# Optimization experiments

Measured on AMD Instinct MI355X. Metric: run time of the kernel, lower is better.

## Reference

```python
import jax, jax.numpy as jnp
import numpy as np

B, T, N_EMBED, HEAD_SIZE = 512, 256, 384, 64

def setup_inputs() -> dict:
    key = jax.random.key(0)
    k1, k2, k3, k4 = jax.random.split(key, 4)
    x = jax.random.normal(k1, (B, T, N_EMBED), dtype=jnp.float32)
    # nn.Linear(n_embed, head_size, bias=False) weights, stored as [in, out] for x @ W
    scale = 1.0 / np.sqrt(N_EMBED)
    Wk = jax.random.uniform(k2, (N_EMBED, HEAD_SIZE), jnp.float32, -scale, scale)
    Wq = jax.random.uniform(k3, (N_EMBED, HEAD_SIZE), jnp.float32, -scale, scale)
    Wv = jax.random.uniform(k4, (N_EMBED, HEAD_SIZE), jnp.float32, -scale, scale)
    return {"x": x, "Wk": Wk, "Wq": Wq, "Wv": Wv}

def reference(x, Wk, Wq, Wv):
    # Single causal self-attention head (dropout in eval mode / identity)
    k = x @ Wk  # [B, T, H]
    q = x @ Wq
    v = x @ Wv
    wei = jnp.einsum('bth,bsh->bts', q, k) * (HEAD_SIZE ** -0.5)  # [B, T, T]
    causal = jnp.tril(jnp.ones((T, T), dtype=bool))
    wei = jnp.where(causal, wei, -jnp.inf)
    wei = jax.nn.softmax(wei, axis=-1)
    out = jnp.einsum('bts,bsh->bth', wei, v)  # [B, T, H]
    return out
```

## Files before the change

### kernel.cpp

```cpp
#include <hip/hip_runtime.h>
#include <stdint.h>


typedef short s16x8 __attribute__((ext_vector_type(8)));
typedef float f32x4 __attribute__((ext_vector_type(4)));

#define LOG2E_OVER_8 0.18033688011112042f

__device__ inline short f2bf(float f) {
  union { float f; uint32_t u; } v; v.f = f;
  uint32_t r = (v.u + 0x7fffu + ((v.u >> 16) & 1u)) >> 16;
  return (short)r;
}

__global__ __launch_bounds__(256) void prep_w(const float* __restrict__ Wk,
                                              const float* __restrict__ Wq,
                                              const float* __restrict__ Wv,
                                              short* __restrict__ Wt2) {
  int idx = blockIdx.x * 256 + threadIdx.x;
  int kk = idx & 31;
  int n = (idx >> 5) % 192;
  int kc = idx / (32 * 192);
  int col = n & 63;
  int w = n >> 6;
  const float* W = (w == 0) ? Wk : (w == 1) ? Wq : Wv;
  float v = W[(kc * 32 + kk) * 64 + col];
  if (w == 1) v *= LOG2E_OVER_8;
  Wt2[idx] = f2bf(v);
}

__global__ __launch_bounds__(256) void qkv_proj(const float* __restrict__ x,
                                                const short* __restrict__ Wt2,
                                                short* __restrict__ Kd,
                                                short* __restrict__ Qd,
                                                short* __restrict__ Vd) {
  __shared__ short Xs[128 * 56];
  __shared__ short Ws[192 * 32];
  const int tid = threadIdx.x;
  const int wave = tid >> 6;
  const int lane = tid & 63;
  const int l15 = lane & 15;
  const int quad = lane >> 4;
  const long m0 = (long)blockIdx.x * 128;

  f32x4 acc[2][12];
#pragma unroll
  for (int mt = 0; mt < 2; ++mt)
#pragma unroll
    for (int n = 0; n < 12; ++n) acc[mt][n] = (f32x4)0.0f;

  const int xrow = tid >> 1;
  const int xcb = (tid & 1) * 16;
  const float* xp0 = x + (m0 + xrow) * 384 + xcb;
  const short* wp0 = Wt2 + tid * 24;
  short* xs = &Xs[xrow * 56 + xcb];
  short* wsp = &Ws[tid * 24];

  for (int kc = 0; kc < 12; ++kc) {
    const float* xp = xp0 + kc * 32;
    f32x4 a0 = *(const f32x4*)(xp);
    f32x4 a1 = *(const f32x4*)(xp + 4);
    f32x4 a2 = *(const f32x4*)(xp + 8);
    f32x4 a3 = *(const f32x4*)(xp + 12);
    const short* wp = wp0 + kc * 6144;
    s16x8 w0 = *(const s16x8*)(wp);
    s16x8 w1 = *(const s16x8*)(wp + 8);
    s16x8 w2 = *(const s16x8*)(wp + 16);

    s16x8 v0, v1;
    v0[0] = f2bf(a0[0]); v0[1] = f2bf(a0[1]); v0[2] = f2bf(a0[2]); v0[3] = f2bf(a0[3]);
    v0[4] = f2bf(a1[0]); v0[5] = f2bf(a1[1]); v0[6] = f2bf(a1[2]); v0[7] = f2bf(a1[3]);
    v1[0] = f2bf(a2[0]); v1[1] = f2bf(a2[1]); v1[2] = f2bf(a2[2]); v1[3] = f2bf(a2[3]);
    v1[4] = f2bf(a3[0]); v1[5] = f2bf(a3[1]); v1[6] = f2bf(a3[2]); v1[7] = f2bf(a3[3]);
    *(s16x8*)xs = v0;
    *(s16x8*)(xs + 8) = v1;
    *(s16x8*)wsp = w0;
    *(s16x8*)(wsp + 8) = w1;
    *(s16x8*)(wsp + 16) = w2;
    __syncthreads();

    s16x8 af0 = *(const s16x8*)&Xs[(wave * 32 + l15) * 56 + quad * 8];
    s16x8 af1 = *(const s16x8*)&Xs[(wave * 32 + 16 + l15) * 56 + quad * 8];
#pragma unroll
    for (int n = 0; n < 12; ++n) {
      s16x8 bf = *(const s16x8*)&Ws[(n * 16 + l15) * 32 + quad * 8];
      acc[0][n] = __builtin_amdgcn_mfma_f32_16x16x32_bf16(af0, bf, acc[0][n], 0, 0, 0);
      acc[1][n] = __builtin_amdgcn_mfma_f32_16x16x32_bf16(af1, bf, acc[1][n], 0, 0, 0);
    }
    __syncthreads();
  }

#pragma unroll
  for (int mt = 0; mt < 2; ++mt) {
    const long rbase = m0 + wave * 32 + mt * 16 + quad * 4;
#pragma unroll
    for (int n = 0; n < 12; ++n) {
      short* dst = (n < 4) ? Kd : (n < 8) ? Qd : Vd;
      const int col = (n & 3) * 16 + l15;
#pragma unroll
      for (int r = 0; r < 4; ++r) {
        dst[(rbase + r) * 64 + col] = f2bf(acc[mt][n][r]);
      }
    }
  }
}

__global__ __launch_bounds__(256) void attn_head(const short* __restrict__ Kd,
                                                 const short* __restrict__ Qd,
                                                 const short* __restrict__ Vd,
                                                 float* __restrict__ out) {
  __shared__ short Ks[64 * 72];
  __shared__ short Vt[64 * 72];
  __shared__ short Ps[4][16 * 72];
  const int tid = threadIdx.x;
  const int wave = tid >> 6;
  const int lane = tid & 63;
  const int l15 = lane & 15;
  const int quad = lane >> 4;
  const int b = blockIdx.x >> 2;
  const int qt = blockIdx.x & 3;
  const short* Kb = Kd + (long)b * (256 * 64);
  const short* Vb = Vd + (long)b * (256 * 64);
  const short* Qb = Qd + (long)b * (256 * 64);

  const int qrow = qt * 64 + wave * 16 + l15;
  s16x8 qf0 = *(const s16x8*)&Qb[qrow * 64 + quad * 8];
  s16x8 qf1 = *(const s16x8*)&Qb[qrow * 64 + 32 + quad * 8];

  f32x4 Oacc[4];
#pragma unroll
  for (int n = 0; n < 4; ++n) Oacc[n] = (f32x4)0.0f;
  float mrow[4] = {-1e30f, -1e30f, -1e30f, -1e30f};
  float lrow[4] = {0.f, 0.f, 0.f, 0.f};

  const int s_row = tid >> 2;
  const int hseg = (tid & 3) * 16;

  for (int c = 0; c <= qt; ++c) {
    const short* kp = Kb + (c * 64 + s_row) * 64 + hseg;
    s16x8 k0 = *(const s16x8*)kp;
    s16x8 k1 = *(const s16x8*)(kp + 8);
    const short* vp = Vb + (c * 64 + s_row) * 64 + hseg;
    s16x8 u0 = *(const s16x8*)vp;
    s16x8 u1 = *(const s16x8*)(vp + 8);
    *(s16x8*)&Ks[s_row * 72 + hseg] = k0;
    *(s16x8*)&Ks[s_row * 72 + hseg + 8] = k1;
#pragma unroll
    for (int i = 0; i < 8; ++i) Vt[(hseg + i) * 72 + s_row] = u0[i];
#pragma unroll
    for (int i = 0; i < 8; ++i) Vt[(hseg + 8 + i) * 72 + s_row] = u1[i];
    __syncthreads();

    f32x4 S[4];
#pragma unroll
    for (int n = 0; n < 4; ++n) {
      s16x8 kf0 = *(const s16x8*)&Ks[(n * 16 + l15) * 72 + quad * 8];
      s16x8 kf1 = *(const s16x8*)&Ks[(n * 16 + l15) * 72 + 32 + quad * 8];
      f32x4 z = (f32x4)0.0f;
      z = __builtin_amdgcn_mfma_f32_16x16x32_bf16(qf0, kf0, z, 0, 0, 0);
      z = __builtin_amdgcn_mfma_f32_16x16x32_bf16(qf1, kf1, z, 0, 0, 0);
      S[n] = z;
    }
    if (c == qt) {
#pragma unroll
      for (int n = 0; n < 4; ++n) {
        int s_loc = n * 16 + l15;
#pragma unroll
        for (int r = 0; r < 4; ++r) {
          int q_loc = wave * 16 + quad * 4 + r;
          if (s_loc > q_loc) S[n][r] = -1e30f;
        }
      }
    }

    float alpha[4];
#pragma unroll
    for (int r = 0; r < 4; ++r) {
      float mx = fmaxf(fmaxf(S[0][r], S[1][r]), fmaxf(S[2][r], S[3][r]));
      mx = fmaxf(mx, __shfl_xor(mx, 1));
      mx = fmaxf(mx, __shfl_xor(mx, 2));
      mx = fmaxf(mx, __shfl_xor(mx, 4));
      mx = fmaxf(mx, __shfl_xor(mx, 8));
      float mnew = fmaxf(mrow[r], mx);
      alpha[r] = __builtin_amdgcn_exp2f(mrow[r] - mnew);
      mrow[r] = mnew;
    }
    float rs[4] = {0.f, 0.f, 0.f, 0.f};
#pragma unroll
    for (int n = 0; n < 4; ++n) {
#pragma unroll
      for (int r = 0; r < 4; ++r) {
        float p = __builtin_amdgcn_exp2f(S[n][r] - mrow[r]);
        rs[r] += p;
        Ps[wave][(quad * 4 + r) * 72 + n * 16 + l15] = f2bf(p);
      }
    }
#pragma unroll
    for (int r = 0; r < 4; ++r) {
      float s = rs[r];
      s += __shfl_xor(s, 1);
      s += __shfl_xor(s, 2);
      s += __shfl_xor(s, 4);
      s += __shfl_xor(s, 8);
      lrow[r] = lrow[r] * alpha[r] + s;
#pragma unroll
      for (int n = 0; n < 4; ++n) Oacc[n][r] *= alpha[r];
    }
    asm volatile("s_waitcnt lgkmcnt(0)" ::: "memory");

    s16x8 pf0 = *(const s16x8*)&Ps[wave][l15 * 72 + quad * 8];
    s16x8 pf1 = *(const s16x8*)&Ps[wave][l15 * 72 + 32 + quad * 8];
#pragma unroll
    for (int n = 0; n < 4; ++n) {
      s16x8 vf0 = *(const s16x8*)&Vt[(n * 16 + l15) * 72 + quad * 8];
      s16x8 vf1 = *(const s16x8*)&Vt[(n * 16 + l15) * 72 + 32 + quad * 8];
      Oacc[n] = __builtin_amdgcn_mfma_f32_16x16x32_bf16(pf0, vf0, Oacc[n], 0, 0, 0);
      Oacc[n] = __builtin_amdgcn_mfma_f32_16x16x32_bf16(pf1, vf1, Oacc[n], 0, 0, 0);
    }
    __syncthreads();
  }

  float inv[4];
#pragma unroll
  for (int r = 0; r < 4; ++r) inv[r] = 1.0f / lrow[r];
  float* ob = out + ((long)b * 256 + qt * 64 + wave * 16 + quad * 4) * 64;
#pragma unroll
  for (int n = 0; n < 4; ++n)
#pragma unroll
    for (int r = 0; r < 4; ++r)
      ob[r * 64 + n * 16 + l15] = Oacc[n][r] * inv[r];
}

extern "C" void kernel_launch(void* const* d_in, const int* in_sizes, int n_in,
                              void* d_out, int out_size, void* d_ws, size_t ws_size,
                              hipStream_t stream) {
  const float* x = (const float*)d_in[0];
  const float* Wk = (const float*)d_in[1];
  const float* Wq = (const float*)d_in[2];
  const float* Wv = (const float*)d_in[3];
  float* out = (float*)d_out;
  char* ws = (char*)d_ws;
  short* Wt2 = (short*)ws;
  short* Kd = (short*)(ws + 147456);
  short* Qd = (short*)(ws + 147456 + 16777216);
  short* Vd = (short*)(ws + 147456 + 2 * 16777216);

  prep_w<<<288, 256, 0, stream>>>(Wk, Wq, Wv, Wt2);
  qkv_proj<<<1024, 256, 0, stream>>>(x, Wt2, Kd, Qd, Vd);
  attn_head<<<2048, 256, 0, stream>>>(Kd, Qd, Vd, out);
}
```

Before: 338.2 us.

## Fuse QKV projection and causal attention into one per-batch kernel

Replaces the separate projection and attention kernels with one kernel per batch element. It computes K, Q and a transposed V for all 256 rows into shared memory and then runs causal flash attention, pairing query tiles (t, 15-t) per wave to balance the causal work. This removes the global round trip of the bf16 K/Q/V intermediates and one kernel launch. In exchange it uses large shared memory per block, launches only 512 blocks, and reads the weight B-fragments directly from global memory instead of staging them in shared memory.

After: 357.3 us. 5.7% more time.

```diff
diff --git a/kernel.cpp b/kernel.cpp
--- a/kernel.cpp
+++ b/kernel.cpp
@@ -3,6 +3,7 @@
 
 
 typedef short s16x8 __attribute__((ext_vector_type(8)));
+typedef short s16x4 __attribute__((ext_vector_type(4)));
 typedef float f32x4 __attribute__((ext_vector_type(4)));
 
 #define LOG2E_OVER_8 0.18033688011112042f
@@ -29,206 +30,171 @@
   Wt2[idx] = f2bf(v);
 }
 
-__global__ __launch_bounds__(256) void qkv_proj(const float* __restrict__ x,
-                                                const short* __restrict__ Wt2,
-                                                short* __restrict__ Kd,
-                                                short* __restrict__ Qd,
-                                                short* __restrict__ Vd) {
-  __shared__ short Xs[128 * 56];
-  __shared__ short Ws[192 * 32];
+__global__ __launch_bounds__(512, 2) void fused_head(const float* __restrict__ x,
+                                                     const short* __restrict__ Wt2,
+                                                     float* __restrict__ out) {
+  __shared__ __align__(16) short Xs[64 * 392];
+  __shared__ __align__(16) short Kls[256 * 72];
+  __shared__ __align__(16) short Qls[256 * 72];
+  __shared__ __align__(16) short Vt[64 * 264];
+
   const int tid = threadIdx.x;
   const int wave = tid >> 6;
   const int lane = tid & 63;
   const int l15 = lane & 15;
   const int quad = lane >> 4;
-  const long m0 = (long)blockIdx.x * 128;
-
-  f32x4 acc[2][12];
-#pragma unroll
-  for (int mt = 0; mt < 2; ++mt)
-#pragma unroll
-    for (int n = 0; n < 12; ++n) acc[mt][n] = (f32x4)0.0f;
-
-  const int xrow = tid >> 1;
-  const int xcb = (tid & 1) * 16;
-  const float* xp0 = x + (m0 + xrow) * 384 + xcb;
-  const short* wp0 = Wt2 + tid * 24;
-  short* xs = &Xs[xrow * 56 + xcb];
-  short* wsp = &Ws[tid * 24];
-
-  for (int kc = 0; kc < 12; ++kc) {
-    const float* xp = xp0 + kc * 32;
-    f32x4 a0 = *(const f32x4*)(xp);
-    f32x4 a1 = *(const f32x4*)(xp + 4);
-    f32x4 a2 = *(const f32x4*)(xp + 8);
-    f32x4 a3 = *(const f32x4*)(xp + 12);
-    const short* wp = wp0 + kc * 6144;
-    s16x8 w0 = *(const s16x8*)(wp);
-    s16x8 w1 = *(const s16x8*)(wp + 8);
-    s16x8 w2 = *(const s16x8*)(wp + 16);
-
-    s16x8 v0, v1;
-    v0[0] = f2bf(a0[0]); v0[1] = f2bf(a0[1]); v0[2] = f2bf(a0[2]); v0[3] = f2bf(a0[3]);
-    v0[4] = f2bf(a1[0]); v0[5] = f2bf(a1[1]); v0[6] = f2bf(a1[2]); v0[7] = f2bf(a1[3]);
-    v1[0] = f2bf(a2[0]); v1[1] = f2bf(a2[1]); v1[2] = f2bf(a2[2]); v1[3] = f2bf(a2[3]);
-    v1[4] = f2bf(a3[0]); v1[5] = f2bf(a3[1]); v1[6] = f2bf(a3[2]); v1[7] = f2bf(a3[3]);
-    *(s16x8*)xs = v0;
-    *(s16x8*)(xs + 8) = v1;
-    *(s16x8*)wsp = w0;
-    *(s16x8*)(wsp + 8) = w1;
-    *(s16x8*)(wsp + 16) = w2;
+  const int b = blockIdx.x;
+  const float* xb = x + (long)b * (256 * 384);
+
+  const int rt = wave >> 1;
+  const int nh = wave & 1;
+  const short* wbase = Wt2 + (nh * 96 + l15) * 32 + quad * 8;
+
+  for (int ch = 0; ch < 4; ++ch) {
+    const int R0 = ch * 64;
+#pragma unroll
+    for (int j = 0; j < 12; ++j) {
+      int slot = tid + j * 512;
+      int row = slot / 96;
+      int c4 = slot - row * 96;
+      f32x4 a = *(const f32x4*)(xb + (R0 + row) * 384 + c4 * 4);
+      s16x4 h;
+      h[0] = f2bf(a[0]); h[1] = f2bf(a[1]); h[2] = f2bf(a[2]); h[3] = f2bf(a[3]);
+      *(s16x4*)&Xs[row * 392 + c4 * 4] = h;
+    }
     __syncthreads();
 
-    s16x8 af0 = *(const s16x8*)&Xs[(wave * 32 + l15) * 56 + quad * 8];
-    s16x8 af1 = *(const s16x8*)&Xs[(wave * 32 + 16 + l15) * 56 + quad * 8];
-#pragma unroll
-    for (int n = 0; n < 12; ++n) {
-      s16x8 bf = *(const s16x8*)&Ws[(n * 16 + l15) * 32 + quad * 8];
-      acc[0][n] = __builtin_amdgcn_mfma_f32_16x16x32_bf16(af0, bf, acc[0][n], 0, 0, 0);
-      acc[1][n] = __builtin_amdgcn_mfma_f32_16x16x32_bf16(af1, bf, acc[1][n], 0, 0, 0);
+    f32x4 acc[6];
+#pragma unroll
+    for (int nt = 0; nt < 6; ++nt) acc[nt] = (f32x4)0.0f;
+    const short* abase = &Xs[(rt * 16 + l15) * 392 + quad * 8];
+#pragma unroll 2
+    for (int kc = 0; kc < 12; ++kc) {
+      s16x8 af = *(const s16x8*)(abase + kc * 32);
+#pragma unroll
+      for (int nt = 0; nt < 6; ++nt) {
+        s16x8 bf = *(const s16x8*)(wbase + kc * 6144 + nt * 512);
+        acc[nt] = __builtin_amdgcn_mfma_f32_16x16x32_bf16(af, bf, acc[nt], 0, 0, 0);
+      }
+    }
+
+    const int srow = R0 + rt * 16 + quad * 4;
+#pragma unroll
+    for (int nt = 0; nt < 6; ++nt) {
+      const int gn = nh * 6 + nt;
+      if (gn < 4) {
+        const int col = gn * 16 + l15;
+#pragma unroll
+        for (int r = 0; r < 4; ++r) Kls[(srow + r) * 72 + col] = f2bf(acc[nt][r]);
+      } else if (gn < 8) {
+        const int col = (gn - 4) * 16 + l15;
+#pragma unroll
+        for (int r = 0; r < 4; ++r) Qls[(srow + r) * 72 + col] = f2bf(acc[nt][r]);
+      } else {
+        const int hcol = (gn - 8) * 16 + l15;
+#pragma unroll
+        for (int r = 0; r < 4; ++r) Vt[hcol * 264 + srow + r] = f2bf(acc[nt][r]);
+      }
     }
     __syncthreads();
   }
 
-#pragma unroll
-  for (int mt = 0; mt < 2; ++mt) {
-    const long rbase = m0 + wave * 32 + mt * 16 + quad * 4;
-#pragma unroll
-    for (int n = 0; n < 12; ++n) {
-      short* dst = (n < 4) ? Kd : (n < 8) ? Qd : Vd;
-      const int col = (n & 3) * 16 + l15;
+  short* Psw = Xs + wave * (16 * 72);
+
+  for (int ti = 0; ti < 2; ++ti) {
+    const int t = ti ? (15 - wave) : wave;
+    const int q0 = t * 16;
+
+    s16x8 qf0 = *(const s16x8*)&Qls[(q0 + l15) * 72 + quad * 8];
+    s16x8 qf1 = *(const s16x8*)&Qls[(q0 + l15) * 72 + 32 + quad * 8];
+
+    f32x4 Oacc[4];
+#pragma unroll
+    for (int n = 0; n < 4; ++n) Oacc[n] = (f32x4)0.0f;
+    float mrow[4] = {-1e30f, -1e30f, -1e30f, -1e30f};
+    float lrow[4] = {0.f, 0.f, 0.f, 0.f};
+
+    const int nchunks = (t >> 2) + 1;
+    for (int c = 0; c < nchunks; ++c) {
+      const int s0 = c * 64;
+      f32x4 S[4];
+#pragma unroll
+      for (int n = 0; n < 4; ++n) {
+        s16x8 kf0 = *(const s16x8*)&Kls[(s0 + n * 16 + l15) * 72 + quad * 8];
+        s16x8 kf1 = *(const s16x8*)&Kls[(s0 + n * 16 + l15) * 72 + 32 + quad * 8];
+        f32x4 z = (f32x4)0.0f;
+        z = __builtin_amdgcn_mfma_f32_16x16x32_bf16(qf0, kf0, z, 0, 0, 0);
+        z = __builtin_amdgcn_mfma_f32_16x16x32_bf16(qf1, kf1, z, 0, 0, 0);
+        S[n] = z;
+      }
+      if (c == nchunks - 1) {
+#pragma unroll
+        for (int n = 0; n < 4; ++n) {
+          const int s_abs = s0 + n * 16 + l15;
+#pragma unroll
+          for (int r = 0; r < 4; ++r) {
+            const int q_abs = q0 + quad * 4 + r;
+            if (s_abs > q_abs) S[n][r] = -1e30f;
+          }
+        }
+      }
+
+      float alpha[4];
 #pragma unroll
       for (int r = 0; r < 4; ++r) {
-        dst[(rbase + r) * 64 + col] = f2bf(acc[mt][n][r]);
-      }
-    }
+        float mx = fmaxf(fmaxf(S[0][r], S[1][r]), fmaxf(S[2][r], S[3][r]));
+        mx = fmaxf(mx, __shfl_xor(mx, 1));
+        mx = fmaxf(mx, __shfl_xor(mx, 2));
+        mx = fmaxf(mx, __shfl_xor(mx, 4));
+        mx = fmaxf(mx, __shfl_xor(mx, 8));
+        float mnew = fmaxf(mrow[r], mx);
+        alpha[r] = __builtin_amdgcn_exp2f(mrow[r] - mnew);
+        mrow[r] = mnew;
+      }
+      float rs[4] = {0.f, 0.f, 0.f, 0.f};
+#pragma unroll
+      for (int n = 0; n < 4; ++n) {
+#pragma unroll
+        for (int r = 0; r < 4; ++r) {
+          float p = __builtin_amdgcn_exp2f(S[n][r] - mrow[r]);
+          rs[r] += p;
+          Psw[(quad * 4 + r) * 72 + n * 16 + l15] = f2bf(p);
+        }
+      }
+#pragma unroll
+      for (int r = 0; r < 4; ++r) {
+        float s = rs[r];
+        s += __shfl_xor(s, 1);
+        s += __shfl_xor(s, 2);
+        s += __shfl_xor(s, 4);
+        s += __shfl_xor(s, 8);
+        lrow[r] = lrow[r] * alpha[r] + s;
+#pragma unroll
+        for (int n = 0; n < 4; ++n) Oacc[n][r] *= alpha[r];
+      }
+      asm volatile("s_waitcnt lgkmcnt(0)" ::: "memory");
+
+      s16x8 pf0 = *(const s16x8*)&Psw[l15 * 72 + quad * 8];
+      s16x8 pf1 = *(const s16x8*)&Psw[l15 * 72 + 32 + quad * 8];
+#pragma unroll
+      for (int n = 0; n < 4; ++n) {
+        s16x8 vf0 = *(const s16x8*)&Vt[(n * 16 + l15) * 264 + s0 + quad * 8];
+        s16x8 vf1 = *(const s16x8*)&Vt[(n * 16 + l15) * 264 + s0 + 32 + quad * 8];
+        Oacc[n] = __builtin_amdgcn_mfma_f32_16x16x32_bf16(pf0, vf0, Oacc[n], 0, 0, 0);
+        Oacc[n] = __builtin_amdgcn_mfma_f32_16x16x32_bf16(pf1, vf1, Oacc[n], 0, 0, 0);
+      }
+    }
+
+    float inv[4];
+#pragma unroll
+    for (int r = 0; r < 4; ++r) inv[r] = 1.0f / lrow[r];
+    float* ob = out + ((long)b * 256 + q0 + quad * 4) * 64;
+#pragma unroll
+    for (int n = 0; n < 4; ++n)
+#pragma unroll
+      for (int r = 0; r < 4; ++r)
+        ob[r * 64 + n * 16 + l15] = Oacc[n][r] * inv[r];
   }
-}
-
-__global__ __launch_bounds__(256) void attn_head(const short* __restrict__ Kd,
-                                                 const short* __restrict__ Qd,
-                                                 const short* __restrict__ Vd,
-                                                 float* __restrict__ out) {
-  __shared__ short Ks[64 * 72];
-  __shared__ short Vt[64 * 72];
-  __shared__ short Ps[4][16 * 72];
-  const int tid = threadIdx.x;
-  const int wave = tid >> 6;
-  const int lane = tid & 63;
-  const int l15 = lane & 15;
-  const int quad = lane >> 4;
-  const int b = blockIdx.x >> 2;
-  const int qt = blockIdx.x & 3;
-  const short* Kb = Kd + (long)b * (256 * 64);
-  const short* Vb = Vd + (long)b * (256 * 64);
-  const short* Qb = Qd + (long)b * (256 * 64);
-
-  const int qrow = qt * 64 + wave * 16 + l15;
-  s16x8 qf0 = *(const s16x8*)&Qb[qrow * 64 + quad * 8];
-  s16x8 qf1 = *(const s16x8*)&Qb[qrow * 64 + 32 + quad * 8];
-
-  f32x4 Oacc[4];
-#pragma unroll
-  for (int n = 0; n < 4; ++n) Oacc[n] = (f32x4)0.0f;
-  float mrow[4] = {-1e30f, -1e30f, -1e30f, -1e30f};
-  float lrow[4] = {0.f, 0.f, 0.f, 0.f};
-
-  const int s_row = tid >> 2;
-  const int hseg = (tid & 3) * 16;
-
-  for (int c = 0; c <= qt; ++c) {
-    const short* kp = Kb + (c * 64 + s_row) * 64 + hseg;
-    s16x8 k0 = *(const s16x8*)kp;
-    s16x8 k1 = *(const s16x8*)(kp + 8);
-    const short* vp = Vb + (c * 64 + s_row) * 64 + hseg;
-    s16x8 u0 = *(const s16x8*)vp;
-    s16x8 u1 = *(const s16x8*)(vp + 8);
-    *(s16x8*)&Ks[s_row * 72 + hseg] = k0;
-    *(s16x8*)&Ks[s_row * 72 + hseg + 8] = k1;
-#pragma unroll
-    for (int i = 0; i < 8; ++i) Vt[(hseg + i) * 72 + s_row] = u0[i];
-#pragma unroll
-    for (int i = 0; i < 8; ++i) Vt[(hseg + 8 + i) * 72 + s_row] = u1[i];
-    __syncthreads();
-
-    f32x4 S[4];
-#pragma unroll
-    for (int n = 0; n < 4; ++n) {
-      s16x8 kf0 = *(const s16x8*)&Ks[(n * 16 + l15) * 72 + quad * 8];
-      s16x8 kf1 = *(const s16x8*)&Ks[(n * 16 + l15) * 72 + 32 + quad * 8];
-      f32x4 z = (f32x4)0.0f;
-      z = __builtin_amdgcn_mfma_f32_16x16x32_bf16(qf0, kf0, z, 0, 0, 0);
-      z = __builtin_amdgcn_mfma_f32_16x16x32_bf16(qf1, kf1, z, 0, 0, 0);
-      S[n] = z;
-    }
-    if (c == qt) {
-#pragma unroll
-      for (int n = 0; n < 4; ++n) {
-        int s_loc = n * 16 + l15;
-#pragma unroll
-        for (int r = 0; r < 4; ++r) {
-          int q_loc = wave * 16 + quad * 4 + r;
-          if (s_loc > q_loc) S[n][r] = -1e30f;
-        }
-      }
-    }
-
-    float alpha[4];
-#pragma unroll
-    for (int r = 0; r < 4; ++r) {
-      float mx = fmaxf(fmaxf(S[0][r], S[1][r]), fmaxf(S[2][r], S[3][r]));
-      mx = fmaxf(mx, __shfl_xor(mx, 1));
-      mx = fmaxf(mx, __shfl_xor(mx, 2));
-      mx = fmaxf(mx, __shfl_xor(mx, 4));
-      mx = fmaxf(mx, __shfl_xor(mx, 8));
-      float mnew = fmaxf(mrow[r], mx);
-      alpha[r] = __builtin_amdgcn_exp2f(mrow[r] - mnew);
-      mrow[r] = mnew;
-    }
-    float rs[4] = {0.f, 0.f, 0.f, 0.f};
-#pragma unroll
-    for (int n = 0; n < 4; ++n) {
-#pragma unroll
-      for (int r = 0; r < 4; ++r) {
-        float p = __builtin_amdgcn_exp2f(S[n][r] - mrow[r]);
-        rs[r] += p;
-        Ps[wave][(quad * 4 + r) * 72 + n * 16 + l15] = f2bf(p);
-      }
-    }
-#pragma unroll
-    for (int r = 0; r < 4; ++r) {
-      float s = rs[r];
-      s += __shfl_xor(s, 1);
-      s += __shfl_xor(s, 2);
-      s += __shfl_xor(s, 4);
-      s += __shfl_xor(s, 8);
-      lrow[r] = lrow[r] * alpha[r] + s;
-#pragma unroll
-      for (int n = 0; n < 4; ++n) Oacc[n][r] *= alpha[r];
-    }
-    asm volatile("s_waitcnt lgkmcnt(0)" ::: "memory");
-
-    s16x8 pf0 = *(const s16x8*)&Ps[wave][l15 * 72 + quad * 8];
-    s16x8 pf1 = *(const s16x8*)&Ps[wave][l15 * 72 + 32 + quad * 8];
-#pragma unroll
-    for (int n = 0; n < 4; ++n) {
-      s16x8 vf0 = *(const s16x8*)&Vt[(n * 16 + l15) * 72 + quad * 8];
-      s16x8 vf1 = *(const s16x8*)&Vt[(n * 16 + l15) * 72 + 32 + quad * 8];
-      Oacc[n] = __builtin_amdgcn_mfma_f32_16x16x32_bf16(pf0, vf0, Oacc[n], 0, 0, 0);
-      Oacc[n] = __builtin_amdgcn_mfma_f32_16x16x32_bf16(pf1, vf1, Oacc[n], 0, 0, 0);
-    }
-    __syncthreads();
-  }
-
-  float inv[4];
-#pragma unroll
-  for (int r = 0; r < 4; ++r) inv[r] = 1.0f / lrow[r];
-  float* ob = out + ((long)b * 256 + qt * 64 + wave * 16 + quad * 4) * 64;
-#pragma unroll
-  for (int n = 0; n < 4; ++n)
-#pragma unroll
-    for (int r = 0; r < 4; ++r)
-      ob[r * 64 + n * 16 + l15] = Oacc[n][r] * inv[r];
 }
 
 extern "C" void kernel_launch(void* const* d_in, const int* in_sizes, int n_in,
@@ -239,13 +205,8 @@
   const float* Wq = (const float*)d_in[2];
   const float* Wv = (const float*)d_in[3];
   float* out = (float*)d_out;
-  char* ws = (char*)d_ws;
-  short* Wt2 = (short*)ws;
-  short* Kd = (short*)(ws + 147456);
-  short* Qd = (short*)(ws + 147456 + 16777216);
-  short* Vd = (short*)(ws + 147456 + 2 * 16777216);
+  short* Wt2 = (short*)d_ws;
 
   prep_w<<<288, 256, 0, stream>>>(Wk, Wq, Wv, Wt2);
-  qkv_proj<<<1024, 256, 0, stream>>>(x, Wt2, Kd, Qd, Vd);
-  attn_head<<<2048, 256, 0, stream>>>(Kd, Qd, Vd, out);
-}
+  fused_head<<<512, 512, 0, stream>>>(x, Wt2, out);
+}
```
